# Kernel tuning notes

Measured on AMD Instinct MI355X. Metric: run time of the kernel, lower is better.

## Reference

```python
import jax, jax.numpy as jnp
import numpy as np

B, T, V, D, H, A = 256, 512, 50000, 256, 256, 128


def setup_inputs() -> dict:
    key = jax.random.key(0)
    ks = jax.random.split(key, 9)
    x = jax.random.randint(ks[0], (B, T), 0, V, dtype=jnp.int32)
    embed_w = jax.random.uniform(ks[1], (V, D), dtype=jnp.float32)          # random_uniform init, non-trainable
    lstm_kernel = jax.random.normal(ks[2], (D + H, 4 * H), dtype=jnp.float32) * 0.05  # BasicLSTMCell kernel [i,j,f,o]
    lstm_bias = jnp.zeros((4 * H,), jnp.float32)
    w_omega = jax.random.normal(ks[3], (H, A), dtype=jnp.float32)
    b_omega = jax.random.normal(ks[4], (A,), dtype=jnp.float32)
    u_omega = jax.random.normal(ks[5], (A,), dtype=jnp.float32)
    w = jax.random.normal(ks[6], (H, 2), dtype=jnp.float32)
    b = jnp.zeros((2,), jnp.float32)
    return {"x": x, "embed_w": embed_w, "lstm_kernel": lstm_kernel,
            "lstm_bias": lstm_bias, "w_omega": w_omega, "b_omega": b_omega,
            "u_omega": u_omega, "w": w, "b": b}


def _lstm_attention_forward(x, embed_w, lstm_kernel, lstm_bias, w_omega, b_omega, u_omega, w, b):
    Bt, Tt = x.shape
    Hh = lstm_bias.shape[0] // 4
    seq_len = jnp.sum(jnp.sign(x), axis=1)                         # [B] like tf.reduce_sum(tf.sign(x))
    e = embed_w[x]                                                  # [B,T,D] embedding lookup
    # dynamic_rnn semantics: outputs zeroed past seq_len, state frozen
    mask = (jnp.arange(Tt)[:, None] < seq_len[None, :]).astype(e.dtype)  # [T,B]
    xs = (jnp.transpose(e, (1, 0, 2)), mask[:, :, None])            # time-major

    def step(carry, inp):
        c, h = carry
        x_t, m = inp                                                # [B,D], [B,1]
        z = jnp.concatenate([x_t, h], axis=-1) @ lstm_kernel + lstm_bias  # [B,4H]
        i, j, f, o = jnp.split(z, 4, axis=-1)
        c_new = c * jax.nn.sigmoid(f + 1.0) + jax.nn.sigmoid(i) * jnp.tanh(j)  # forget_bias=1.0
        h_new = jnp.tanh(c_new) * jax.nn.sigmoid(o)
        c = jnp.where(m > 0, c_new, c)
        h_out = h_new * m
        h = jnp.where(m > 0, h_new, h)
        return (c, h), h_out

    c0 = jnp.zeros((Bt, Hh), e.dtype)
    h0 = jnp.zeros((Bt, Hh), e.dtype)
    _, outs = jax.lax.scan(step, (c0, h0), xs)                      # [T,B,H]
    outs = jnp.transpose(outs, (1, 0, 2))                           # [B,T,H]

    # additive attention pooling
    value = jnp.tanh(jnp.einsum('bth,ha->bta', outs, w_omega) + b_omega)
    vu = jnp.einsum('bta,a->bt', value, u_omega)
    alphas = jax.nn.softmax(vu, axis=-1)                            # [B,T]
    last = jnp.sum(outs * alphas[..., None], axis=1)                # [B,H]

    logits = last @ w + b                                           # [B,2]
    return jax.nn.softmax(logits)


def reference(x, embed_w, lstm_kernel, lstm_bias, w_omega, b_omega, u_omega, w, b):
    return _lstm_attention_forward(x, embed_w, lstm_kernel, lstm_bias,
                                   w_omega, b_omega, u_omega, w, b)
```

## Files before the change

kernel.cpp:

```cpp
#include <hip/hip_runtime.h>
#include <hip/hip_bf16.h>
#include <cstdint>
#include <cstddef>

typedef _Float16 f16;
typedef _Float16 f16x8 __attribute__((ext_vector_type(8)));
typedef _Float16 f16x4 __attribute__((ext_vector_type(4)));
typedef float f32x4 __attribute__((ext_vector_type(4)));
typedef unsigned long long u64;
typedef unsigned int u32;

#define B_   256
#define T_   512
#define V_   50000
#define D_   256
#define H_   256
#define A_   128
#define N4H  1024

__device__ __forceinline__ float sigmoid_f(float x) {
    return __builtin_amdgcn_rcpf(1.f + __expf(-x));
}
__device__ __forceinline__ float tanh_f(float x) {
    float e = __expf(-2.f * fabsf(x));
    float t = 1.f - 2.f * e * __builtin_amdgcn_rcpf(1.f + e);
    return copysignf(t, x);
}

#define MFMA_A(accv, afragv, bfraga)                                         \
    asm volatile("v_mfma_f32_16x16x32_f16 %0, %1, %2, %0"                    \
                 : "+v"(accv) : "v"(afragv), "a"(bfraga))

#define LGKM_BARRIER()                                                       \
    do {                                                                     \
        asm volatile("s_waitcnt lgkmcnt(0)" ::: "memory");                   \
        __builtin_amdgcn_sched_barrier(0);                                   \
        __builtin_amdgcn_s_barrier();                                        \
        __builtin_amdgcn_sched_barrier(0);                                   \
    } while (0)

__global__ __launch_bounds__(256) void k0_convert(
    const float* __restrict__ lstm_kernel, const float* __restrict__ w_omega,
    f16* __restrict__ WxT, f16* __restrict__ WhT, f16* __restrict__ WomT) {
    int blk = blockIdx.x;
    int tau = threadIdx.x;
    if (blk < N4H) {
        int n = blk;
        WxT[n * 256 + tau] = (f16)lstm_kernel[(size_t)tau * N4H + n];
        WhT[n * 256 + tau] = (f16)lstm_kernel[(size_t)(256 + tau) * N4H + n];
    } else {
        int a = blk - N4H;
        WomT[a * 256 + tau] = (f16)w_omega[(size_t)tau * A_ + a];
    }
}

__global__ __launch_bounds__(256) void k1_seqlen(
    const int* __restrict__ x, int* __restrict__ seqlen) {
    __shared__ int red[256];
    int b = blockIdx.x, tau = threadIdx.x;
    int cnt = (x[b * T_ + tau] != 0) + (x[b * T_ + tau + 256] != 0);
    red[tau] = cnt;
    __syncthreads();
    for (int s = 128; s > 0; s >>= 1) {
        if (tau < s) red[tau] += red[tau + s];
        __syncthreads();
    }
    if (tau == 0) seqlen[b] = red[0];
}

__global__ __launch_bounds__(256) void k2_zx(
    const int* __restrict__ x, const float* __restrict__ embed,
    const f16* __restrict__ WxT, const float* __restrict__ bias,
    f16* __restrict__ Zx, int t0, int Tc) {
    __shared__ __align__(16) f16 A_s[64][264];
    __shared__ __align__(16) f16 B_s[128][72];
    __shared__ int tok_s[64];

    int tau  = threadIdx.x;
    int bm   = blockIdx.x;
    int i0   = bm * 64;
    int wave = tau >> 6, lane = tau & 63;
    int q = lane >> 4, c = lane & 15;

    if (tau < 64) {
        int i  = i0 + tau;
        int bb = i / Tc, tr = i - bb * Tc;
        tok_s[tau] = x[bb * T_ + t0 + tr];
    }
    __syncthreads();

    {
        int r = tau >> 2, quarter = tau & 3;
        const float4* src =
            (const float4*)(embed + (size_t)tok_s[r] * D_ + quarter * 64);
        f16* dst = &A_s[r][quarter * 64];
#pragma unroll
        for (int j = 0; j < 16; j++) {
            float4 v = src[j];
            dst[j * 4 + 0] = (f16)v.x;
            dst[j * 4 + 1] = (f16)v.y;
            dst[j * 4 + 2] = (f16)v.z;
            dst[j * 4 + 3] = (f16)v.w;
        }
    }

    for (int np = 0; np < 8; np++) {
        f32x4 acc[8];
#pragma unroll
        for (int ni = 0; ni < 8; ni++) acc[ni] = (f32x4){0.f, 0.f, 0.f, 0.f};

        for (int kt = 0; kt < 4; kt++) {
            __syncthreads();
            {
                int n = tau >> 1, half = tau & 1;
                const f16x8* src = (const f16x8*)(WxT +
                    (size_t)(np * 128 + n) * 256 + kt * 64 + half * 32);
                f16x8* dst = (f16x8*)&B_s[n][half * 32];
#pragma unroll
                for (int j = 0; j < 4; j++) dst[j] = src[j];
            }
            __syncthreads();
#pragma unroll
            for (int s = 0; s < 2; s++) {
                f16x8 afrag =
                    *(const f16x8*)&A_s[wave * 16 + c][kt * 64 + s * 32 + q * 8];
#pragma unroll
                for (int ni = 0; ni < 8; ni++) {
                    f16x8 bfrag = *(const f16x8*)&B_s[ni * 16 + c][s * 32 + q * 8];
                    acc[ni] = __builtin_amdgcn_mfma_f32_16x16x32_f16(
                        afrag, bfrag, acc[ni], 0, 0, 0);
                }
            }
        }
#pragma unroll
        for (int ni = 0; ni < 8; ni++) {
            int n    = np * 128 + ni * 16 + c;
            int g    = n >> 8, rem = n & 255;
            int half = rem >> 7, colu = rem & 127;
            int np2  = half * 512 + colu * 4 + g;
            float bv = bias[n];
#pragma unroll
            for (int r = 0; r < 4; r++) {
                int row = i0 + wave * 16 + q * 4 + r;
                Zx[(size_t)row * N4H + np2] = (f16)(acc[ni][r] + bv);
            }
        }
    }
}

__device__ __forceinline__ void zx_producer(
    const int* __restrict__ x, const float* __restrict__ embed,
    const f16* __restrict__ WxT, const float* __restrict__ bias,
    f16* __restrict__ Zx, int pb, int t0, int Tc) {
    __shared__ __align__(16) f16 Ap_s[128][264];
    __shared__ __align__(16) f16 Bp_s[128][72];
    __shared__ int tokp_s[128];

    int tau  = threadIdx.x;
    int i0   = pb * 128;
    int wave = tau >> 6, lane = tau & 63;
    int q = lane >> 4, c = lane & 15;

    if (tau < 128) {
        int i  = i0 + tau;
        int bb = i / Tc, tr = i - bb * Tc;
        tokp_s[tau] = x[bb * T_ + t0 + tr];
    }
    __syncthreads();

    {
        int r = tau >> 2, quarter = tau & 3;
        const float4* src =
            (const float4*)(embed + (size_t)tokp_s[r] * D_ + quarter * 64);
        f16* dst = &Ap_s[r][quarter * 64];
#pragma unroll
        for (int j = 0; j < 16; j++) {
            float4 v = src[j];
            dst[j * 4 + 0] = (f16)v.x;
            dst[j * 4 + 1] = (f16)v.y;
            dst[j * 4 + 2] = (f16)v.z;
            dst[j * 4 + 3] = (f16)v.w;
        }
    }

    for (int np = 0; np < 8; np++) {
        f32x4 acc[8];
#pragma unroll
        for (int ni = 0; ni < 8; ni++) acc[ni] = (f32x4){0.f, 0.f, 0.f, 0.f};

        for (int kt = 0; kt < 4; kt++) {
            __syncthreads();
            {
                int n = tau >> 2, qt = tau & 3;
                const f16x8* src = (const f16x8*)(WxT +
                    (size_t)(np * 128 + n) * 256 + kt * 64 + qt * 16);
                f16x8* dst = (f16x8*)&Bp_s[n][qt * 16];
                dst[0] = src[0];
                dst[1] = src[1];
            }
            __syncthreads();
#pragma unroll
            for (int s = 0; s < 2; s++) {
                f16x8 afrag =
                    *(const f16x8*)&Ap_s[wave * 16 + c][kt * 64 + s * 32 + q * 8];
#pragma unroll
                for (int ni = 0; ni < 8; ni++) {
                    f16x8 bfrag = *(const f16x8*)&Bp_s[ni * 16 + c][s * 32 + q * 8];
                    acc[ni] = __builtin_amdgcn_mfma_f32_16x16x32_f16(
                        afrag, bfrag, acc[ni], 0, 0, 0);
                }
            }
        }
#pragma unroll
        for (int ni = 0; ni < 8; ni++) {
            int n     = np * 128 + ni * 16 + c;
            int g     = n >> 8, rem = n & 255;
            int halfn = rem >> 7, colu = rem & 127;
            int np2   = halfn * 512 + colu * 4 + g;
            float bv  = bias[n];
#pragma unroll
            for (int r = 0; r < 4; r++) {
                int row = i0 + wave * 16 + q * 4 + r;
                Zx[(size_t)row * N4H + np2] = (f16)(acc[ni][r] + bv);
            }
        }
    }
}

__global__ __launch_bounds__(512, 2) void k3_lstm(
    const f16* __restrict__ Zx, const f16* __restrict__ WhT,
    const int* __restrict__ seqlen, f16* __restrict__ outs,
    f16* __restrict__ Hstate, float* __restrict__ Cstate,
    u32* __restrict__ Hex, int t0, int Tc, int first, int last,
    const int* __restrict__ x, const float* __restrict__ embed,
    const f16* __restrict__ WxT, const float* __restrict__ bias,
    f16* __restrict__ ZxNext, int t0n) {
    if (blockIdx.x >= 32) {
        zx_producer(x, embed, WxT, bias, ZxNext, blockIdx.x - 32, t0n, Tc);
        return;
    }

    __shared__ __align__(16) f16 Zx_s[2][16][520];
    __shared__ __align__(16) f16 h_s[2][16][264];

    int tau  = threadIdx.x;
    int w    = tau >> 6, lane = tau & 63;
    int q = lane >> 4, c = lane & 15;
    int wgid = blockIdx.x;
    int pair = wgid >> 1, half = wgid & 1;
    int b0 = pair * 16;
    int u0 = half * 128, pu0 = (half ^ 1) * 128;
    int u  = u0 + w * 16 + c;
    int col = w * 16 + c;

    u32* hexw_my = Hex + (size_t)wgid * 2 * 2048;
    u32* hexw_pr = Hex + (size_t)(wgid ^ 1) * 2 * 2048;

    f32x4 wha[4][8];
#pragma unroll
    for (int g = 0; g < 4; g++)
#pragma unroll
        for (int s = 0; s < 8; s++) {
            int kc = (s < 4) ? (half * 4 + s) : ((half ^ 1) * 4 + (s - 4));
            f16x8 f = *(const f16x8*)(WhT +
                (size_t)(g * 256 + u0 + w * 16 + c) * 256 + kc * 32 + q * 8);
            f32x4 t = __builtin_bit_cast(f32x4, f);
            asm volatile("" : "=a"(wha[g][s]) : "0"(t));
        }

    int kOwn = half * 128 + q * 8;
    int kPar = (half ^ 1) * 128 + q * 8;

    int p0 = t0 & 1;
    if (first) {
        for (int idx = tau; idx < 2 * 16 * 264; idx += 512)
            ((f16*)h_s)[idx] = (f16)0.f;
    } else {
        for (int idx = tau; idx < 16 * 256; idx += 512) {
            int r = idx >> 8, k = idx & 255;
            h_s[p0][r][k] = Hstate[(b0 + r) * H_ + k];
        }
    }

    float cst[4];
    f16   hprev[4];
    int   sl[4];
#pragma unroll
    for (int r = 0; r < 4; r++) {
        int row = q * 4 + r;
        cst[r]   = first ? 0.f : Cstate[(b0 + row) * H_ + u];
        hprev[r] = first ? (f16)0.f : Hstate[(b0 + row) * H_ + u];
        sl[r]    = seqlen[b0 + row];
    }

    int r_st = tau >> 5;
    int cc   = (tau & 31) * 16;
    const f16* zxrow = Zx + ((size_t)(b0 + r_st) * Tc) * N4H + half * 512 + cc;

    {
        const f16x8* src = (const f16x8*)zxrow;
        f16x8* dst = (f16x8*)&Zx_s[p0][r_st][cc];
        dst[0] = src[0];
        dst[1] = src[1];
    }
    int rr = tau >> 5;
    int uu = (tau & 31) * 4;

    __syncthreads();

    f32x4 accO[4];
#pragma unroll
    for (int g = 0; g < 4; g++) accO[g] = (f32x4){0.f, 0.f, 0.f, 0.f};
#pragma unroll
    for (int kk = 0; kk < 4; kk++) {
        f16x8 afrag = *(const f16x8*)&h_s[p0][c][kOwn + kk * 32];
#pragma unroll
        for (int g = 0; g < 4; g++) MFMA_A(accO[g], afrag, wha[g][kk]);
    }

    u64 vp0 = 0, vp1 = 0;

    for (int tt = 0; tt < Tc; tt++) {
        int t   = t0 + tt;
        int cur = t & 1, nxt = cur ^ 1;

        int tn = (tt + 1 < Tc) ? tt + 1 : tt;
        const f16x8* psrc = (const f16x8*)(zxrow + (size_t)tn * N4H);
        f16x8 z0 = psrc[0];
        f16x8 z1 = psrc[1];

        if (tt > 0) {
            u32 tagp = (u32)(t & 0xffff);
            const u64* pp = (const u64*)&hexw_pr[cur * 2048 + rr * 128 + uu];
            while (((u32)(vp0 >> 16) & 0xffffu) != tagp ||
                   ((u32)(vp0 >> 48)) != tagp ||
                   ((u32)(vp1 >> 16) & 0xffffu) != tagp ||
                   ((u32)(vp1 >> 48)) != tagp) {
                vp0 = __hip_atomic_load(pp + 0, __ATOMIC_RELAXED,
                                        __HIP_MEMORY_SCOPE_AGENT);
                vp1 = __hip_atomic_load(pp + 1, __ATOMIC_RELAXED,
                                        __HIP_MEMORY_SCOPE_AGENT);
            }
            u64 hw = (u64)(vp0 & 0xffff) | (((vp0 >> 32) & 0xffff) << 16) |
                     ((vp1 & 0xffff) << 32) | (((vp1 >> 32) & 0xffff) << 48);
            *(u64*)&h_s[cur][rr][pu0 + uu] = hw;
        }
        LGKM_BARRIER();

#pragma unroll
        for (int kk = 0; kk < 4; kk++) {
            f16x8 afrag = *(const f16x8*)&h_s[cur][c][kPar + kk * 32];
#pragma unroll
            for (int g = 0; g < 4; g++) MFMA_A(accO[g], afrag, wha[g][4 + kk]);
        }

        u32 tag = (u32)((t + 1) & 0xffff);
        f16 ovals[4];
#pragma unroll
        for (int r = 0; r < 4; r++) {
            int row = q * 4 + r;
            f16x4 zv = *(const f16x4*)&Zx_s[cur][row][col * 4];
            float zi = accO[0][r] + (float)zv[0];
            float zj = accO[1][r] + (float)zv[1];
            float zf = accO[2][r] + (float)zv[2];
            float zo = accO[3][r] + (float)zv[3];
            float ig = sigmoid_f(zi);
            float jg = tanh_f(zj);
            float fg = sigmoid_f(zf + 1.f);
            float og = sigmoid_f(zo);
            float cn = cst[r] * fg + ig * jg;
            float hn = tanh_f(cn) * og;
            bool  m  = (t < sl[r]);
            cst[r]   = m ? cn : cst[r];
            f16 hkeep = m ? (f16)hn : hprev[r];
            hprev[r]  = hkeep;
            h_s[nxt][row][u] = hkeep;
            u32 word = (tag << 16) |
                       (u32)(unsigned short)__builtin_bit_cast(short, hkeep);
            __hip_atomic_store(&hexw_my[nxt * 2048 + row * 128 + col], word,
                               __ATOMIC_RELAXED, __HIP_MEMORY_SCOPE_AGENT);
            ovals[r] = m ? (f16)hn : (f16)0.f;
        }

        {
            f16x8* dst = (f16x8*)&Zx_s[nxt][r_st][cc];
            dst[0] = z0;
            dst[1] = z1;
        }

#pragma unroll
        for (int r = 0; r < 4; r++)
            outs[((size_t)(b0 + q * 4 + r) * T_ + t) * H_ + u] = ovals[r];

        {
            const u64* pp2 = (const u64*)&hexw_pr[nxt * 2048 + rr * 128 + uu];
            vp0 = __hip_atomic_load(pp2 + 0, __ATOMIC_RELAXED,
                                    __HIP_MEMORY_SCOPE_AGENT);
            vp1 = __hip_atomic_load(pp2 + 1, __ATOMIC_RELAXED,
                                    __HIP_MEMORY_SCOPE_AGENT);
        }

        LGKM_BARRIER();

#pragma unroll
        for (int g = 0; g < 4; g++) accO[g] = (f32x4){0.f, 0.f, 0.f, 0.f};
#pragma unroll
        for (int kk = 0; kk < 4; kk++) {
            f16x8 afrag = *(const f16x8*)&h_s[nxt][c][kOwn + kk * 32];
#pragma unroll
            for (int g = 0; g < 4; g++) MFMA_A(accO[g], afrag, wha[g][kk]);
        }
    }

    if (!last) {
        int parity = (t0 + Tc) & 1;
        for (int idx = tau; idx < 16 * 128; idx += 512) {
            int r = idx >> 7, k = u0 + (idx & 127);
            Hstate[(b0 + r) * H_ + k] = h_s[parity][r][k];
        }
#pragma unroll
        for (int r = 0; r < 4; r++)
            Cstate[(b0 + q * 4 + r) * H_ + u] = cst[r];
    }
}

__global__ __launch_bounds__(256) void k4_attn(
    const f16* __restrict__ outs, const f16* __restrict__ WomT,
    const float* __restrict__ b_omega, const float* __restrict__ u_omega,
    const float* __restrict__ w, const float* __restrict__ bfin,
    float* __restrict__ out) {
    __shared__ __align__(16) f16 A_s[64][264];
    __shared__ __align__(16) f16 val_s[64][132];
    __shared__ float u_s[128];
    __shared__ float vu_s[512];
    __shared__ float red0[256], red1[256];

    int b = blockIdx.x, tau = threadIdx.x;
    int wave = tau >> 6, lane = tau & 63;
    int q = lane >> 4, c = lane & 15;

    if (tau < 128) u_s[tau] = u_omega[tau];
    float bom[8];
#pragma unroll
    for (int ni = 0; ni < 8; ni++) bom[ni] = b_omega[ni * 16 + c];

    for (int ch = 0; ch < 8; ch++) {
        int t0c = ch * 64;
        __syncthreads();
        {
            int r = tau >> 2, seg = tau & 3;
            const f16x8* src =
                (const f16x8*)(outs + ((size_t)b * T_ + t0c + r) * H_ + seg * 64);
            f16x8* dst = (f16x8*)&A_s[r][seg * 64];
#pragma unroll
            for (int j = 0; j < 8; j++) dst[j] = src[j];
        }
        __syncthreads();

        f32x4 acc[8];
#pragma unroll
        for (int ni = 0; ni < 8; ni++) acc[ni] = (f32x4){0.f, 0.f, 0.f, 0.f};
#pragma unroll
        for (int kc = 0; kc < 8; kc++) {
            f16x8 afrag = *(const f16x8*)&A_s[wave * 16 + c][kc * 32 + q * 8];
#pragma unroll
            for (int ni = 0; ni < 8; ni++) {
                f16x8 bfrag = *(const f16x8*)(WomT +
                    (size_t)(ni * 16 + c) * 256 + kc * 32 + q * 8);
                acc[ni] = __builtin_amdgcn_mfma_f32_16x16x32_f16(
                    afrag, bfrag, acc[ni], 0, 0, 0);
            }
        }
#pragma unroll
        for (int ni = 0; ni < 8; ni++) {
#pragma unroll
            for (int r = 0; r < 4; r++) {
                val_s[wave * 16 + q * 4 + r][ni * 16 + c] =
                    (f16)tanh_f(acc[ni][r] + bom[ni]);
            }
        }
        __syncthreads();
        if (tau < 64) {
            float s = 0.f;
#pragma unroll 8
            for (int a = 0; a < 128; a++) s += (float)val_s[tau][a] * u_s[a];
            vu_s[t0c + tau] = s;
        }
    }
    __syncthreads();

    red0[tau] = fmaxf(vu_s[tau], vu_s[tau + 256]);
    __syncthreads();
    for (int s = 128; s > 0; s >>= 1) {
        if (tau < s) red0[tau] = fmaxf(red0[tau], red0[tau + s]);
        __syncthreads();
    }
    float mx = red0[0];
    __syncthreads();
    float e0 = __expf(vu_s[tau] - mx), e1 = __expf(vu_s[tau + 256] - mx);
    red0[tau] = e0 + e1;
    __syncthreads();
    for (int s = 128; s > 0; s >>= 1) {
        if (tau < s) red0[tau] += red0[tau + s];
        __syncthreads();
    }
    float inv = 1.f / red0[0];
    __syncthreads();
    vu_s[tau]       = e0 * inv;
    vu_s[tau + 256] = e1 * inv;
    __syncthreads();

    float lastv = 0.f;
#pragma unroll 4
    for (int t = 0; t < T_; t++)
        lastv += vu_s[t] * (float)outs[((size_t)b * T_ + t) * H_ + tau];

    red0[tau] = lastv * w[tau * 2 + 0];
    red1[tau] = lastv * w[tau * 2 + 1];
    __syncthreads();
    for (int s = 128; s > 0; s >>= 1) {
        if (tau < s) {
            red0[tau] += red0[tau + s];
            red1[tau] += red1[tau + s];
        }
        __syncthreads();
    }
    if (tau == 0) {
        float l0 = red0[0] + bfin[0], l1 = red1[0] + bfin[1];
        float mm = fmaxf(l0, l1);
        float a0 = __expf(l0 - mm), a1 = __expf(l1 - mm);
        float den = a0 + a1;
        out[b * 2 + 0] = a0 / den;
        out[b * 2 + 1] = a1 / den;
    }
}

extern "C" void kernel_launch(void* const* d_in, const int* in_sizes, int n_in,
                              void* d_out, int out_size, void* d_ws,
                              size_t ws_size, hipStream_t stream) {
    const int*   x           = (const int*)d_in[0];
    const float* embed       = (const float*)d_in[1];
    const float* lstm_kernel = (const float*)d_in[2];
    const float* lstm_bias   = (const float*)d_in[3];
    const float* w_omega     = (const float*)d_in[4];
    const float* b_omega     = (const float*)d_in[5];
    const float* u_omega     = (const float*)d_in[6];
    const float* w           = (const float*)d_in[7];
    const float* bfin        = (const float*)d_in[8];
    float*       out         = (float*)d_out;

    char* ws = (char*)d_ws;
    f16*   WxT    = (f16*)(ws + 0);
    f16*   WhT    = (f16*)(ws + 524288);
    f16*   WomT   = (f16*)(ws + 1048576);
    int*   seqlen = (int*)(ws + 1114112);
    f16*   Hstate = (f16*)(ws + 1115136);
    float* Cstate = (float*)(ws + 1246208);
    u32*   Hex    = (u32*)(ws + 1508352);
    f16*   outs   = (f16*)(ws + 2032640);

    const size_t fixed = 2032640ull + 67108864ull;
    int nch = 1;
    while (nch < 16 && fixed + 2ull * (268435456ull / (size_t)nch) > ws_size)
        nch <<= 1;
    int Tc = T_ / nch;
    size_t chunkB = 268435456ull / (size_t)nch;
    f16* ZxA = (f16*)(ws + fixed);
    f16* ZxB = (f16*)(ws + fixed + chunkB);

    k0_convert<<<1152, 256, 0, stream>>>(lstm_kernel, w_omega, WxT, WhT, WomT);
    k1_seqlen<<<256, 256, 0, stream>>>(x, seqlen);
    k2_zx<<<(B_ * Tc) / 64, 256, 0, stream>>>(x, embed, WxT, lstm_bias, ZxA,
                                              0, Tc);
    for (int chk = 0; chk < nch; chk++) {
        int  t0  = chk * Tc;
        f16* zc  = (chk & 1) ? ZxB : ZxA;
        f16* zn  = (chk & 1) ? ZxA : ZxB;
        int  np  = (chk + 1 < nch) ? (B_ * Tc) / 128 : 0;
        int  t0n = (chk + 1) * Tc;
        k3_lstm<<<32 + np, 512, 0, stream>>>(
            zc, WhT, seqlen, outs, Hstate, Cstate, Hex, t0, Tc,
            chk == 0 ? 1 : 0, chk == nch - 1 ? 1 : 0,
            x, embed, WxT, lstm_bias, zn, t0n);
    }
    k4_attn<<<256, 256, 0, stream>>>(outs, WomT, b_omega, u_omega, w, bfin, out);
}
```

Before: 1.447 ms.

## Overlap attention score computation with LSTM recurrence using extra producer blocks

Adds vu_producer blocks to the chunked LSTM kernel that compute the attention scores (tanh(outs·W_omega+b)·u) for the previous time chunk while the recurrence runs on the current one. The final attention kernel then only computes scores for the last chunk and reads the rest from a workspace buffer. Shared memory is unified into one raw buffer reused by the recurrence, Zx producer and vu producer roles. It only activates when the workspace forces multiple chunks, and the extra blocks may compete with the latency-critical recurrence blocks for CUs and bandwidth.

Measured after the change: 1.443 ms. About the same (-0.3%).

```diff
diff --git a/kernel.cpp b/kernel.cpp
--- a/kernel.cpp
+++ b/kernel.cpp
@@ -148,13 +148,15 @@
     }
 }
 
+#define SMEM_BYTES 87040
+
 __device__ __forceinline__ void zx_producer(
     const int* __restrict__ x, const float* __restrict__ embed,
     const f16* __restrict__ WxT, const float* __restrict__ bias,
-    f16* __restrict__ Zx, int pb, int t0, int Tc) {
-    __shared__ __align__(16) f16 Ap_s[128][264];
-    __shared__ __align__(16) f16 Bp_s[128][72];
-    __shared__ int tokp_s[128];
+    f16* __restrict__ Zx, int pb, int t0, int Tc, char* smem) {
+    f16 (*Ap_s)[264] = (f16(*)[264])smem;
+    f16 (*Bp_s)[72]  = (f16(*)[72])(smem + 67584);
+    int* tokp_s      = (int*)(smem + 86016);
 
     int tau  = threadIdx.x;
     int i0   = pb * 128;
@@ -227,6 +229,70 @@
     }
 }
 
+__device__ __forceinline__ void vu_producer(
+    const f16* __restrict__ outs, const f16* __restrict__ WomT,
+    const float* __restrict__ b_omega, const float* __restrict__ u_omega,
+    float* __restrict__ vuout, int b, int t0v, int Tc, char* smem) {
+    f16 (*A_s)[264]   = (f16(*)[264])smem;
+    f16 (*val_s)[132] = (f16(*)[132])(smem + 33792);
+    float* u_s        = (float*)(smem + 50688);
+
+    int tau  = threadIdx.x;
+    int wave = tau >> 6, lane = tau & 63;
+    int q = lane >> 4, c = lane & 15;
+
+    if (tau < 128) u_s[tau] = u_omega[tau];
+    float bom[8];
+#pragma unroll
+    for (int ni = 0; ni < 8; ni++) bom[ni] = b_omega[ni * 16 + c];
+
+    int nchap = Tc >> 6;
+    for (int ch = 0; ch < nchap; ch++) {
+        int t0c = t0v + ch * 64;
+        __syncthreads();
+        if (tau < 256) {
+            int r = tau >> 2, seg = tau & 3;
+            const f16x8* src =
+                (const f16x8*)(outs + ((size_t)b * T_ + t0c + r) * H_ + seg * 64);
+            f16x8* dst = (f16x8*)&A_s[r][seg * 64];
+#pragma unroll
+            for (int j = 0; j < 8; j++) dst[j] = src[j];
+        }
+        __syncthreads();
+        if (tau < 256) {
+            f32x4 acc[8];
+#pragma unroll
+            for (int ni = 0; ni < 8; ni++) acc[ni] = (f32x4){0.f, 0.f, 0.f, 0.f};
+#pragma unroll
+            for (int kc = 0; kc < 8; kc++) {
+                f16x8 afrag = *(const f16x8*)&A_s[wave * 16 + c][kc * 32 + q * 8];
+#pragma unroll
+                for (int ni = 0; ni < 8; ni++) {
+                    f16x8 bfrag = *(const f16x8*)(WomT +
+                        (size_t)(ni * 16 + c) * 256 + kc * 32 + q * 8);
+                    acc[ni] = __builtin_amdgcn_mfma_f32_16x16x32_f16(
+                        afrag, bfrag, acc[ni], 0, 0, 0);
+                }
+            }
+#pragma unroll
+            for (int ni = 0; ni < 8; ni++) {
+#pragma unroll
+                for (int r = 0; r < 4; r++) {
+                    val_s[wave * 16 + q * 4 + r][ni * 16 + c] =
+                        (f16)tanh_f(acc[ni][r] + bom[ni]);
+                }
+            }
+        }
+        __syncthreads();
+        if (tau < 64) {
+            float s = 0.f;
+#pragma unroll 8
+            for (int a = 0; a < 128; a++) s += (float)val_s[tau][a] * u_s[a];
+            vuout[(size_t)b * T_ + t0c + tau] = s;
+        }
+    }
+}
+
 __global__ __launch_bounds__(512, 2) void k3_lstm(
     const f16* __restrict__ Zx, const f16* __restrict__ WhT,
     const int* __restrict__ seqlen, f16* __restrict__ outs,
@@ -234,14 +300,23 @@
     u32* __restrict__ Hex, int t0, int Tc, int first, int last,
     const int* __restrict__ x, const float* __restrict__ embed,
     const f16* __restrict__ WxT, const float* __restrict__ bias,
-    f16* __restrict__ ZxNext, int t0n) {
+    f16* __restrict__ ZxNext, int t0n, int npz,
+    const f16* __restrict__ WomT, const float* __restrict__ b_omega,
+    const float* __restrict__ u_omega, float* __restrict__ vuout, int t0v) {
+    __shared__ __align__(16) char smem[SMEM_BYTES];
+
     if (blockIdx.x >= 32) {
-        zx_producer(x, embed, WxT, bias, ZxNext, blockIdx.x - 32, t0n, Tc);
+        int pid = blockIdx.x - 32;
+        if (pid < npz)
+            zx_producer(x, embed, WxT, bias, ZxNext, pid, t0n, Tc, smem);
+        else
+            vu_producer(outs, WomT, b_omega, u_omega, vuout, pid - npz, t0v,
+                        Tc, smem);
         return;
     }
 
-    __shared__ __align__(16) f16 Zx_s[2][16][520];
-    __shared__ __align__(16) f16 h_s[2][16][264];
+    f16 (*Zx_s)[16][520] = (f16(*)[16][520])smem;
+    f16 (*h_s)[16][264]  = (f16(*)[16][264])(smem + 33280);
 
     int tau  = threadIdx.x;
     int w    = tau >> 6, lane = tau & 63;
@@ -428,7 +503,7 @@
     const f16* __restrict__ outs, const f16* __restrict__ WomT,
     const float* __restrict__ b_omega, const float* __restrict__ u_omega,
     const float* __restrict__ w, const float* __restrict__ bfin,
-    float* __restrict__ out) {
+    const float* __restrict__ vuin, int tstart, float* __restrict__ out) {
     __shared__ __align__(16) f16 A_s[64][264];
     __shared__ __align__(16) f16 val_s[64][132];
     __shared__ float u_s[128];
@@ -444,7 +519,9 @@
 #pragma unroll
     for (int ni = 0; ni < 8; ni++) bom[ni] = b_omega[ni * 16 + c];
 
-    for (int ch = 0; ch < 8; ch++) {
+    for (int t = tau; t < tstart; t += 256) vu_s[t] = vuin[(size_t)b * T_ + t];
+
+    for (int ch = tstart >> 6; ch < 8; ch++) {
         int t0c = ch * 64;
         __syncthreads();
         {
@@ -557,9 +634,10 @@
     f16*   Hstate = (f16*)(ws + 1115136);
     float* Cstate = (float*)(ws + 1246208);
     u32*   Hex    = (u32*)(ws + 1508352);
-    f16*   outs   = (f16*)(ws + 2032640);
-
-    const size_t fixed = 2032640ull + 67108864ull;
+    float* vu     = (float*)(ws + 2032640);
+    f16*   outs   = (f16*)(ws + 2556928);
+
+    const size_t fixed = 2556928ull + 67108864ull;
     int nch = 1;
     while (nch < 16 && fixed + 2ull * (268435456ull / (size_t)nch) > ws_size)
         nch <<= 1;
@@ -567,6 +645,9 @@
     size_t chunkB = 268435456ull / (size_t)nch;
     f16* ZxA = (f16*)(ws + fixed);
     f16* ZxB = (f16*)(ws + fixed + chunkB);
+
+    int vuEnable = (Tc % 64 == 0) && (nch >= 2);
+    int tstart   = vuEnable ? (nch - 1) * Tc : 0;
 
     k0_convert<<<1152, 256, 0, stream>>>(lstm_kernel, w_omega, WxT, WhT, WomT);
     k1_seqlen<<<256, 256, 0, stream>>>(x, seqlen);
@@ -576,12 +657,16 @@
         int  t0  = chk * Tc;
         f16* zc  = (chk & 1) ? ZxB : ZxA;
         f16* zn  = (chk & 1) ? ZxA : ZxB;
-        int  np  = (chk + 1 < nch) ? (B_ * Tc) / 128 : 0;
+        int  npz = (chk + 1 < nch) ? (B_ * Tc) / 128 : 0;
+        int  nv  = (vuEnable && chk >= 1) ? B_ : 0;
         int  t0n = (chk + 1) * Tc;
-        k3_lstm<<<32 + np, 512, 0, stream>>>(
+        int  t0v = (chk - 1) * Tc;
+        k3_lstm<<<32 + npz + nv, 512, 0, stream>>>(
             zc, WhT, seqlen, outs, Hstate, Cstate, Hex, t0, Tc,
             chk == 0 ? 1 : 0, chk == nch - 1 ? 1 : 0,
-            x, embed, WxT, lstm_bias, zn, t0n);
-    }
-    k4_attn<<<256, 256, 0, stream>>>(outs, WomT, b_omega, u_omega, w, bfin, out);
-}
+            x, embed, WxT, lstm_bias, zn, t0n, npz,
+            WomT, b_omega, u_omega, vu, t0v);
+    }
+    k4_attn<<<256, 256, 0, stream>>>(outs, WomT, b_omega, u_omega, w, bfin,
+                                     vu, tstart, out);
+}
```
